# Performance work log

Hardware: AMD Instinct MI355X
Metric: run time of the kernel (lower is better)

## Reference

```python
import jax, jax.numpy as jnp
import numpy as np

N_HEAD = 16
HEAD_DIM = 64
N_EMBD = N_HEAD * HEAD_DIM  # 1024


def setup_inputs() -> dict:
    key = jax.random.key(0)
    ks = jax.random.split(key, 5)
    B, S = 2, 2048
    x = jax.random.normal(ks[0], (B, S, N_EMBD), dtype=jnp.float32)
    qkv_w = jax.random.normal(ks[1], (N_EMBD, 3 * N_EMBD), dtype=jnp.float32) * 0.02
    qkv_b = jax.random.normal(ks[2], (3 * N_EMBD,), dtype=jnp.float32) * 0.02
    proj_w = jax.random.normal(ks[3], (N_EMBD, N_EMBD), dtype=jnp.float32) * 0.02
    proj_b = jax.random.normal(ks[4], (N_EMBD,), dtype=jnp.float32) * 0.02
    return {"x": x, "qkv_w": qkv_w, "qkv_b": qkv_b, "proj_w": proj_w, "proj_b": proj_b}


def reference(x, qkv_w, qkv_b, proj_w, proj_b):
    B, S, _ = x.shape
    qkv = x @ qkv_w + qkv_b  # [B,S,3E]
    q, k, v = jnp.split(qkv, 3, axis=-1)
    # [B,H,S,D]
    q = q.reshape(B, S, N_HEAD, HEAD_DIM).transpose(0, 2, 1, 3)
    k = k.reshape(B, S, N_HEAD, HEAD_DIM).transpose(0, 2, 1, 3)
    v = v.reshape(B, S, N_HEAD, HEAD_DIM).transpose(0, 2, 1, 3)
    scale = 1.0 / jnp.sqrt(jnp.float32(HEAD_DIM))
    scores = jnp.einsum('bhqd,bhkd->bhqk', q, k) * scale  # [B,H,S,S]
    causal = jnp.tril(jnp.ones((S, S), dtype=bool))
    scores = jnp.where(causal[None, None], scores, jnp.float32(-jnp.inf))
    attn = jax.nn.softmax(scores, axis=-1)  # dropout p=0 (eval)
    out = jnp.einsum('bhqk,bhkd->bhqd', attn, v)
    out = out.transpose(0, 2, 1, 3).reshape(B, S, N_EMBD)
    out = out @ proj_w + proj_b  # resid dropout p=0
    return out, k, v
```

## Files before the change

kernel.cpp:

```cpp
#include <hip/hip_runtime.h>
#include <hip/hip_bf16.h>


typedef __attribute__((ext_vector_type(4))) float f32x4;
typedef __attribute__((ext_vector_type(16))) float f32x16;
typedef __attribute__((ext_vector_type(8))) short s16x8;
typedef __attribute__((ext_vector_type(4))) short s16x4;

__device__ __forceinline__ short f2bf(float f) {
    union { float f; unsigned u; } x{f};
    unsigned r = x.u + 0x7fff + ((x.u >> 16) & 1);
    return (short)(r >> 16);
}

__device__ __forceinline__ void gload_lds16(const void* g, void* l) {
    __builtin_amdgcn_global_load_lds(
        (const __attribute__((address_space(1))) void*)g,
        (__attribute__((address_space(3))) void*)l, 16, 0, 0);
}

__global__ __launch_bounds__(256) void fused_prepass(const float* __restrict__ x,
                                                     short* __restrict__ x_bf,
                                                     const float* __restrict__ qkv_w,
                                                     short* __restrict__ wT1,
                                                     const float* __restrict__ proj_w,
                                                     short* __restrict__ wT2) {
    __shared__ float tile[32][33];
    const int bid = blockIdx.x, tid = threadIdx.x;
    if (bid < 2048) {
        int i = (bid * 256 + tid) * 8;
        f32x4 a = *(const f32x4*)&x[i];
        f32x4 b = *(const f32x4*)&x[i + 4];
        s16x8 o;
        #pragma unroll
        for (int j = 0; j < 4; ++j) o[j] = f2bf(a[j]);
        #pragma unroll
        for (int j = 0; j < 4; ++j) o[j + 4] = f2bf(b[j]);
        *(s16x8*)&x_bf[i] = o;
        return;
    }
    const float* in;
    short* out;
    int K = 1024, N, n0, k0;
    if (bid < 5120) {
        int blk = bid - 2048;
        in = qkv_w; out = wT1; N = 3072;
        n0 = (blk % 96) * 32; k0 = (blk / 96) * 32;
    } else {
        int blk = bid - 5120;
        in = proj_w; out = wT2; N = 1024;
        n0 = (blk & 31) * 32; k0 = (blk >> 5) * 32;
    }
    const int tx = tid & 31, ty = tid >> 5;
    #pragma unroll
    for (int r = 0; r < 4; ++r)
        tile[ty + r * 8][tx] = in[(long)(k0 + ty + r * 8) * N + n0 + tx];
    __syncthreads();
    #pragma unroll
    for (int r = 0; r < 4; ++r)
        out[(long)(n0 + ty + r * 8) * K + k0 + tx] = f2bf(tile[tx][ty + r * 8]);
}

__global__ __launch_bounds__(256) void gemm1_bf16(
    const short* __restrict__ A, const short* __restrict__ Bt,
    const float* __restrict__ bias, int M, int N, int K,
    short* __restrict__ qbf, short* __restrict__ kbf, short* __restrict__ vbfT,
    float* __restrict__ kout, float* __restrict__ vout) {
    __shared__ __align__(16) short As[128 * 64];
    __shared__ __align__(16) short Bs[128 * 64];
    const int tid = threadIdx.x;
    const int l = tid & 63, w = tid >> 6;
    const int lr = l >> 4, lc = l & 15;
    const int wm = w >> 1, wn = w & 1;
    const int bid = blockIdx.x;
    const int xcd = bid & 7, s = bid >> 3;
    const int bx = (xcd & 1) * 12 + s % 12, by = (xcd >> 1) * 8 + s / 12;
    const int m0 = by * 128, n0 = bx * 128;

    f32x4 acc[4][4] = {};

    for (int kb = 0; kb < K; kb += 64) {
        __syncthreads();
        #pragma unroll
        for (int j = 0; j < 4; ++j) {
            const int c = tid + 256 * j;
            const int row = c >> 3;
            const int lseg = (c & 7) ^ (row & 7);
            gload_lds16(A + (long)(m0 + row) * K + kb + lseg * 8, As + c * 8);
            gload_lds16(Bt + (long)(n0 + row) * K + kb + lseg * 8, Bs + c * 8);
        }
        __syncthreads();
        #pragma unroll
        for (int kh = 0; kh < 2; ++kh) {
            s16x8 af[4], bfr[4];
            #pragma unroll
            for (int mi = 0; mi < 4; ++mi) {
                const int row = wm * 64 + mi * 16 + lc;
                af[mi] = *(const s16x8*)&As[row * 64 + (((kh * 4 + lr) ^ (lc & 7)) * 8)];
            }
            #pragma unroll
            for (int ni = 0; ni < 4; ++ni) {
                const int row = wn * 64 + ni * 16 + lc;
                bfr[ni] = *(const s16x8*)&Bs[row * 64 + (((kh * 4 + lr) ^ (lc & 7)) * 8)];
            }
            #pragma unroll
            for (int mi = 0; mi < 4; ++mi)
                #pragma unroll
                for (int ni = 0; ni < 4; ++ni)
                    acc[mi][ni] = __builtin_amdgcn_mfma_f32_16x16x32_bf16(
                        af[mi], bfr[ni], acc[mi][ni], 0, 0, 0);
        }
    }

    #pragma unroll
    for (int mi = 0; mi < 4; ++mi) {
        #pragma unroll
        for (int ni = 0; ni < 4; ++ni) {
            int col = n0 + wn * 64 + ni * 16 + lc;
            float bv = bias[col];
            int sec = col >> 10, rem = col & 1023;
            int h = rem >> 6, d = rem & 63;
            int row0 = m0 + wm * 64 + mi * 16 + lr * 4;
            int b = row0 >> 11, s0 = row0 & 2047;
            long idxSD = ((long)((b << 4) + h) * 2048 + s0) * 64 + d;
            if (sec == 0) {
                #pragma unroll
                for (int i = 0; i < 4; ++i) {
                    float val = acc[mi][ni][i] + bv;
                    qbf[idxSD + (long)i * 64] = f2bf(val * 0.1803368801111244f);
                }
            } else if (sec == 1) {
                #pragma unroll
                for (int i = 0; i < 4; ++i) {
                    float val = acc[mi][ni][i] + bv;
                    kout[idxSD + (long)i * 64] = val;
                    kbf[idxSD + (long)i * 64] = f2bf(val);
                }
            } else {
                s16x4 pk;
                #pragma unroll
                for (int i = 0; i < 4; ++i) {
                    float val = acc[mi][ni][i] + bv;
                    vout[idxSD + (long)i * 64] = val;
                    pk[i] = f2bf(val);
                }
                *(s16x4*)&vbfT[((long)((b << 4) + h) * 64 + d) * 2048 + s0] = pk;
            }
        }
    }
}

__global__ __launch_bounds__(512) void gemm2_bf16(
    const short* __restrict__ A, const short* __restrict__ Bt,
    const float* __restrict__ bias, int M, int N, int K,
    float* __restrict__ outf) {
    __shared__ __align__(16) short As[2][128 * 64];
    __shared__ __align__(16) short Bs[2][128 * 64];
    const int tid = threadIdx.x;
    const int l = tid & 63, wv = tid >> 6;
    const int grp = wv >> 2, w = wv & 3;
    const int lr = l >> 4, lc = l & 15;
    const int wm = w >> 1, wn = w & 1;
    const int bid = blockIdx.x;
    const int xcd = bid & 7, s = bid >> 3;
    const int bx = (xcd & 1) * 4 + (s & 3), by = (xcd >> 1) * 8 + (s >> 2);
    const int m0 = by * 128, n0 = bx * 128;
    const int gtid = tid & 255;

    f32x4 acc[4][4] = {};

    for (int it = 0; it < 8; ++it) {
        const int kb = grp * 512 + it * 64;
        __syncthreads();
        #pragma unroll
        for (int j = 0; j < 4; ++j) {
            const int c = gtid + 256 * j;
            const int row = c >> 3;
            const int lseg = (c & 7) ^ (row & 7);
            gload_lds16(A + (long)(m0 + row) * K + kb + lseg * 8, &As[grp][c * 8]);
            gload_lds16(Bt + (long)(n0 + row) * K + kb + lseg * 8, &Bs[grp][c * 8]);
        }
        __syncthreads();
        #pragma unroll
        for (int kh = 0; kh < 2; ++kh) {
            s16x8 af[4], bfr[4];
            #pragma unroll
            for (int mi = 0; mi < 4; ++mi) {
                const int row = wm * 64 + mi * 16 + lc;
                af[mi] = *(const s16x8*)&As[grp][row * 64 + (((kh * 4 + lr) ^ (lc & 7)) * 8)];
            }
            #pragma unroll
            for (int ni = 0; ni < 4; ++ni) {
                const int row = wn * 64 + ni * 16 + lc;
                bfr[ni] = *(const s16x8*)&Bs[grp][row * 64 + (((kh * 4 + lr) ^ (lc & 7)) * 8)];
            }
            #pragma unroll
            for (int mi = 0; mi < 4; ++mi)
                #pragma unroll
                for (int ni = 0; ni < 4; ++ni)
                    acc[mi][ni] = __builtin_amdgcn_mfma_f32_16x16x32_bf16(
                        af[mi], bfr[ni], acc[mi][ni], 0, 0, 0);
        }
    }

    __syncthreads();
    float* reg = (w < 2) ? (float*)&As[w][0] : (float*)&Bs[w - 2][0];
    if (grp == 1) {
        #pragma unroll
        for (int mi = 0; mi < 4; ++mi)
            #pragma unroll
            for (int ni = 0; ni < 4; ++ni)
                #pragma unroll
                for (int i = 0; i < 4; ++i)
                    reg[(mi * 16 + lr * 4 + i) * 64 + ni * 16 + lc] = acc[mi][ni][i];
    }
    __syncthreads();
    if (grp == 1) return;
    #pragma unroll
    for (int mi = 0; mi < 4; ++mi)
        #pragma unroll
        for (int ni = 0; ni < 4; ++ni)
            #pragma unroll
            for (int i = 0; i < 4; ++i)
                acc[mi][ni][i] += reg[(mi * 16 + lr * 4 + i) * 64 + ni * 16 + lc];

    #pragma unroll
    for (int mi = 0; mi < 4; ++mi) {
        #pragma unroll
        for (int ni = 0; ni < 4; ++ni) {
            int col = n0 + wn * 64 + ni * 16 + lc;
            float bv = bias[col];
            #pragma unroll
            for (int i = 0; i < 4; ++i) {
                int row = m0 + wm * 64 + mi * 16 + lr * 4 + i;
                outf[(long)row * N + col] = acc[mi][ni][i] + bv;
            }
        }
    }
}

__global__ __launch_bounds__(512, 4) void attn_kernel(const short* __restrict__ qbf,
                                                      const short* __restrict__ kbf,
                                                      const short* __restrict__ vbfT,
                                                      short* __restrict__ obf) {
    const int bid = blockIdx.x;
    const int xcd = bid & 7, r = bid >> 3;
    const int head_local = r & 3, q16 = r >> 2;
    const int qt = (q16 < 8) ? (q16 + 8) : (15 - q16);
    const int bh = xcd * 4 + head_local;
    const int tid = threadIdx.x;
    const int wv = tid >> 6, l = tid & 63;
    const int strip = wv & 3, kh = wv >> 2;
    const int h = l >> 5;
    const int l8 = l & 7;
    const int q0 = qt * 128 + strip * 32;
    const int qlane = q0 + (l & 31);
    const long baseSD = (long)bh * 2048 * 64;
    const long baseDS = (long)bh * 64 * 2048;

    __shared__ __align__(16) short Ks[2][64 * 64];
    __shared__ __align__(16) short Vs[2][64 * 64];
    __shared__ __align__(16) float MG[4][64][36];

    const int sSub = l >> 3;
    const int sChunk = (l & 7) ^ sSub;
    auto stage = [&](int kt, int nb) {
        const int k0 = kt * 64;
        const int r0 = wv * 8 + sSub;
        gload_lds16(kbf + baseSD + (long)(k0 + r0) * 64 + sChunk * 8,
                    &Ks[nb][(wv * 8) * 64]);
        gload_lds16(vbfT + baseDS + (long)r0 * 2048 + k0 + sChunk * 8,
                    &Vs[nb][(wv * 8) * 64]);
    };

    s16x8 qf[4];
    #pragma unroll
    for (int dd = 0; dd < 4; ++dd)
        qf[dd] = *(const s16x8*)&qbf[baseSD + (long)qlane * 64 + dd * 16 + h * 8];

    f32x4 lacc = {};
    f32x16 O[2] = {};

    const int nkt = 2 * qt + 2;

    stage(0, 0);
    __syncthreads();
    int cur = 0;

    for (int kt = 0; kt < nkt; ++kt) {
        if (kt + 1 < nkt) stage(kt + 1, cur ^ 1);
        const int kbase = kt * 64 + kh * 32;

        if (kbase <= q0 + 31) {
            const short* Kb = Ks[cur];
            const short* Vb = Vs[cur];
            f32x16 z = {};
            #pragma unroll
            for (int dd = 0; dd < 4; ++dd) {
                s16x8 kf = *(const s16x8*)&Kb[(kh * 32 + (l & 31)) * 64 +
                                              (((2 * dd + h) ^ l8) * 8)];
                z = __builtin_amdgcn_mfma_f32_32x32x16_bf16(kf, qf[dd], z, 0, 0, 0);
            }
            if (kbase + 31 > q0) {
                #pragma unroll
                for (int rr = 0; rr < 16; ++rr) {
                    int kpos = kbase + (rr & 3) + 8 * (rr >> 2) + 4 * h;
                    if (kpos > qlane) z[rr] = -INFINITY;
                }
            }
            float p[16];
            #pragma unroll
            for (int rr = 0; rr < 16; ++rr) {
                p[rr] = __builtin_amdgcn_exp2f(z[rr]);
                lacc[rr & 3] += p[rr];
            }
            #pragma unroll
            for (int f = 0; f < 2; ++f) {
                union { __hip_bfloat162 b2[4]; s16x8 v; } pk;
                #pragma unroll
                for (int j = 0; j < 4; ++j)
                    pk.b2[j] = __float22bfloat162_rn(
                        make_float2(p[f * 8 + 2 * j], p[f * 8 + 2 * j + 1]));
                const int c0 = kh * 4 + f * 2;
                #pragma unroll
                for (int dt2 = 0; dt2 < 2; ++dt2) {
                    const short* vr = &Vb[(dt2 * 32 + (l & 31)) * 64];
                    s16x8 vf;
                    *(s16x4*)&vf = *(const s16x4*)&vr[(c0 ^ l8) * 8 + 4 * h];
                    *(((s16x4*)&vf) + 1) = *(const s16x4*)&vr[((c0 + 1) ^ l8) * 8 + 4 * h];
                    O[dt2] = __builtin_amdgcn_mfma_f32_32x32x16_bf16(vf, pk.v,
                                                                     O[dt2], 0, 0, 0);
                }
            }
        }
        __syncthreads();
        cur ^= 1;
    }

    float lsum = (lacc[0] + lacc[1]) + (lacc[2] + lacc[3]);
    if (kh == 1) {
        float* row = &MG[strip][l][0];
        #pragma unroll
        for (int dt2 = 0; dt2 < 2; ++dt2)
            #pragma unroll
            for (int rr = 0; rr < 16; ++rr)
                row[dt2 * 16 + rr] = O[dt2][rr];
        row[32] = lsum;
    }
    __syncthreads();
    if (kh == 0) {
        const float* row = &MG[strip][l][0];
        lsum += row[32];
        lsum += __shfl_xor(lsum, 32);
        const int b = bh >> 4, hd = bh & 15;
        float inv = 1.0f / lsum;
        #pragma unroll
        for (int dt2 = 0; dt2 < 2; ++dt2) {
            #pragma unroll
            for (int g = 0; g < 4; ++g) {
                s16x4 o;
                #pragma unroll
                for (int i = 0; i < 4; ++i)
                    o[i] = f2bf((O[dt2][g * 4 + i] + row[dt2 * 16 + g * 4 + i]) * inv);
                const int d = dt2 * 32 + 8 * g + 4 * h;
                *(s16x4*)&obf[(long)(b * 2048 + qlane) * 1024 + hd * 64 + d] = o;
            }
        }
    }
}


extern "C" void kernel_launch(void* const* d_in, const int* in_sizes, int n_in,
                              void* d_out, int out_size, void* d_ws, size_t ws_size,
                              hipStream_t stream) {
    const float* x = (const float*)d_in[0];
    const float* qkv_w = (const float*)d_in[1];
    const float* qkv_b = (const float*)d_in[2];
    const float* proj_w = (const float*)d_in[3];
    const float* proj_b = (const float*)d_in[4];

    float* out = (float*)d_out;
    float* kout = out + 4194304;
    float* vout = out + 8388608;

    short* x_bf = (short*)d_ws;
    short* wT1 = x_bf + 4194304;
    short* wT2 = wT1 + 3145728;
    short* q_bf = wT2 + 1048576;
    short* k_bf = q_bf + 4194304;
    short* vT_bf = k_bf + 4194304;
    short* o_bf = x_bf;

    fused_prepass<<<6144, 256, 0, stream>>>(x, x_bf, qkv_w, wT1, proj_w, wT2);

    gemm1_bf16<<<768, 256, 0, stream>>>(x_bf, wT1, qkv_b, 4096, 3072, 1024,
                                        q_bf, k_bf, vT_bf, kout, vout);

    attn_kernel<<<512, 512, 0, stream>>>(q_bf, k_bf, vT_bf, o_bf);

    gemm2_bf16<<<256, 512, 0, stream>>>(o_bf, wT2, proj_b, 4096, 1024, 1024, out);
}
```

Measured before the change: 99.69 us.

## Split K across two wave groups in QKV GEMM with LDS reduction

The QKV projection GEMM now launches 512 threads per block. Two groups of four waves each compute half of the K dimension into separate LDS buffers, and group 1 then writes its partial accumulators into LDS for group 0 to add before the epilogue. This doubles the waves per tile and halves the serial K loop, which should help latency hiding in a grid of only 768 blocks. The cost is twice the LDS footprint, an extra reduction pass through LDS, and group 1 sitting idle during the epilogue.

After: 112.4 us. +12.7%, slower.

```diff
diff --git a/kernel.cpp b/kernel.cpp
--- a/kernel.cpp
+++ b/kernel.cpp
@@ -61,33 +61,36 @@
         out[(long)(n0 + ty + r * 8) * K + k0 + tx] = f2bf(tile[tx][ty + r * 8]);
 }
 
-__global__ __launch_bounds__(256) void gemm1_bf16(
+__global__ __launch_bounds__(512) void gemm1_bf16(
     const short* __restrict__ A, const short* __restrict__ Bt,
     const float* __restrict__ bias, int M, int N, int K,
     short* __restrict__ qbf, short* __restrict__ kbf, short* __restrict__ vbfT,
     float* __restrict__ kout, float* __restrict__ vout) {
-    __shared__ __align__(16) short As[128 * 64];
-    __shared__ __align__(16) short Bs[128 * 64];
+    __shared__ __align__(16) short As[2][128 * 64];
+    __shared__ __align__(16) short Bs[2][128 * 64];
     const int tid = threadIdx.x;
-    const int l = tid & 63, w = tid >> 6;
+    const int l = tid & 63, wv = tid >> 6;
+    const int grp = wv >> 2, w = wv & 3;
     const int lr = l >> 4, lc = l & 15;
     const int wm = w >> 1, wn = w & 1;
     const int bid = blockIdx.x;
     const int xcd = bid & 7, s = bid >> 3;
     const int bx = (xcd & 1) * 12 + s % 12, by = (xcd >> 1) * 8 + s / 12;
     const int m0 = by * 128, n0 = bx * 128;
+    const int gtid = tid & 255;
 
     f32x4 acc[4][4] = {};
 
-    for (int kb = 0; kb < K; kb += 64) {
+    for (int it = 0; it < 8; ++it) {
+        const int kb = grp * 512 + it * 64;
         __syncthreads();
         #pragma unroll
         for (int j = 0; j < 4; ++j) {
-            const int c = tid + 256 * j;
+            const int c = gtid + 256 * j;
             const int row = c >> 3;
             const int lseg = (c & 7) ^ (row & 7);
-            gload_lds16(A + (long)(m0 + row) * K + kb + lseg * 8, As + c * 8);
-            gload_lds16(Bt + (long)(n0 + row) * K + kb + lseg * 8, Bs + c * 8);
+            gload_lds16(A + (long)(m0 + row) * K + kb + lseg * 8, &As[grp][c * 8]);
+            gload_lds16(Bt + (long)(n0 + row) * K + kb + lseg * 8, &Bs[grp][c * 8]);
         }
         __syncthreads();
         #pragma unroll
@@ -96,12 +99,12 @@
             #pragma unroll
             for (int mi = 0; mi < 4; ++mi) {
                 const int row = wm * 64 + mi * 16 + lc;
-                af[mi] = *(const s16x8*)&As[row * 64 + (((kh * 4 + lr) ^ (lc & 7)) * 8)];
+                af[mi] = *(const s16x8*)&As[grp][row * 64 + (((kh * 4 + lr) ^ (lc & 7)) * 8)];
             }
             #pragma unroll
             for (int ni = 0; ni < 4; ++ni) {
                 const int row = wn * 64 + ni * 16 + lc;
-                bfr[ni] = *(const s16x8*)&Bs[row * 64 + (((kh * 4 + lr) ^ (lc & 7)) * 8)];
+                bfr[ni] = *(const s16x8*)&Bs[grp][row * 64 + (((kh * 4 + lr) ^ (lc & 7)) * 8)];
             }
             #pragma unroll
             for (int mi = 0; mi < 4; ++mi)
@@ -111,6 +114,27 @@
                         af[mi], bfr[ni], acc[mi][ni], 0, 0, 0);
         }
     }
+
+    __syncthreads();
+    float* reg = (w < 2) ? (float*)&As[w][0] : (float*)&Bs[w - 2][0];
+    if (grp == 1) {
+        #pragma unroll
+        for (int mi = 0; mi < 4; ++mi)
+            #pragma unroll
+            for (int ni = 0; ni < 4; ++ni)
+                #pragma unroll
+                for (int i = 0; i < 4; ++i)
+                    reg[(mi * 16 + lr * 4 + i) * 64 + ni * 16 + lc] = acc[mi][ni][i];
+    }
+    __syncthreads();
+    if (grp == 1) return;
+    #pragma unroll
+    for (int mi = 0; mi < 4; ++mi)
+        #pragma unroll
+        for (int ni = 0; ni < 4; ++ni)
+            #pragma unroll
+            for (int i = 0; i < 4; ++i)
+                acc[mi][ni][i] += reg[(mi * 16 + lr * 4 + i) * 64 + ni * 16 + lc];
 
     #pragma unroll
     for (int mi = 0; mi < 4; ++mi) {
@@ -393,7 +417,7 @@
 
     fused_prepass<<<6144, 256, 0, stream>>>(x, x_bf, qkv_w, wT1, proj_w, wT2);
 
-    gemm1_bf16<<<768, 256, 0, stream>>>(x_bf, wT1, qkv_b, 4096, 3072, 1024,
+    gemm1_bf16<<<768, 512, 0, stream>>>(x_bf, wT1, qkv_b, 4096, 3072, 1024,
                                         q_bf, k_bf, vT_bf, kout, vout);
 
     attn_kernel<<<512, 512, 0, stream>>>(q_bf, k_bf, vT_bf, o_bf);
```
